# Kernel optimization log

Hardware: AMD Instinct MI355X
Metric: run time of the kernel (lower is better)

Reference implementation:

```python
import jax, jax.numpy as jnp
import numpy as np

NUM_EXPERTS = 8
TOP_K = 2


def setup_inputs() -> dict:
    key = jax.random.key(0)
    k1, k2 = jax.random.split(key)
    N, D = 8192, 4096
    inputs = jax.random.normal(k1, (N, D), dtype=jnp.float32)
    # torch.nn.Linear weight is [out_features, in_features] = [E, D]
    gate_w = jax.random.normal(k2, (NUM_EXPERTS, D), dtype=jnp.float32) * (1.0 / np.sqrt(D))
    return {"inputs": inputs, "gate_w": gate_w}


def reference(inputs, gate_w):
    # gate linear (no bias): [N, D] x [D, E] -> [N, E]
    router_logits = jnp.einsum("nd,ed->ne", inputs.astype(jnp.float32), gate_w)
    router_weights = jax.nn.softmax(router_logits, axis=1)
    # top-k over experts, renormalize selected weights
    sel_w, sel_idx = jax.lax.top_k(router_weights, TOP_K)          # [N, K]
    sel_w = sel_w / jnp.sum(sel_w, axis=-1, keepdims=True)
    # dense equivalent of the per-expert torch.where dispatch:
    # combine[n, e] = renormalized weight of token n for expert e (0 if not selected).
    onehot = jax.nn.one_hot(sel_idx, NUM_EXPERTS, dtype=sel_w.dtype)  # [N, K, E]
    combine = jnp.einsum("nk,nke->ne", sel_w, onehot)               # [N, E]
    return combine, sel_idx
```

## Files before the change

### kernel.cpp

```cpp
#include <hip/hip_runtime.h>
#include <math.h>

#define N_TOK 8192
#define DIM   4096
#define NEXP  8
#define TPW   4
#define HALF  (DIM / 2)
#define ITERS (HALF / 256)
#define WS_NEED ((size_t)N_TOK * 2 * NEXP * sizeof(float))

__global__ __launch_bounds__(256) void router_part_kernel(
    const float* __restrict__ x,
    const float* __restrict__ w,
    float* __restrict__ part)
{
    __shared__ float wl[NEXP][HALF];

    const int tid  = threadIdx.x;
    const int lane = tid & 63;
    const int wid  = tid >> 6;
    const int h    = blockIdx.x & 1;
    const int blk  = blockIdx.x >> 1;
    const int n0   = blk * 16 + wid * TPW;

    {
        const float* wsrc = w + h * HALF;
        #pragma unroll
        for (int e = 0; e < NEXP; ++e) {
            #pragma unroll
            for (int p = 0; p < 2; ++p) {
                const int pos = p * 1024 + tid * 4;
                const float4 v = *(const float4*)(wsrc + (size_t)e * DIM + pos);
                *(float4*)&wl[e][pos] = v;
            }
        }
    }
    __syncthreads();

    const float* xr = x + (size_t)n0 * DIM + h * HALF + lane * 4;
    float4 xq[ITERS][TPW];
    #pragma unroll
    for (int j = 0; j < ITERS; ++j)
        #pragma unroll
        for (int t = 0; t < TPW; ++t)
            xq[j][t] = *(const float4*)(xr + (size_t)t * DIM + j * 256);

    float acc[TPW][NEXP];
    #pragma unroll
    for (int t = 0; t < TPW; ++t)
        #pragma unroll
        for (int e = 0; e < NEXP; ++e) acc[t][e] = 0.0f;

    #pragma unroll
    for (int j = 0; j < ITERS; ++j) {
        float4 wv[NEXP];
        #pragma unroll
        for (int e = 0; e < NEXP; ++e)
            wv[e] = *(const float4*)&wl[e][j * 256 + lane * 4];
        #pragma unroll
        for (int t = 0; t < TPW; ++t) {
            const float4 xv = xq[j][t];
            #pragma unroll
            for (int e = 0; e < NEXP; ++e) {
                acc[t][e] = fmaf(xv.x, wv[e].x,
                            fmaf(xv.y, wv[e].y,
                            fmaf(xv.z, wv[e].z,
                            fmaf(xv.w, wv[e].w, acc[t][e]))));
            }
        }
    }

    #pragma unroll
    for (int t = 0; t < TPW; ++t) {
        #pragma unroll
        for (int e = 0; e < NEXP; ++e) {
            float v = acc[t][e];
            #pragma unroll
            for (int off = 32; off >= 1; off >>= 1)
                v += __shfl_xor(v, off, 64);
            acc[t][e] = v;
        }
    }

    if (lane == 0) {
        #pragma unroll
        for (int t = 0; t < TPW; ++t) {
            float* p = part + ((size_t)(n0 + t) * 2 + h) * NEXP;
            *(float4*)(p + 0) = make_float4(acc[t][0], acc[t][1], acc[t][2], acc[t][3]);
            *(float4*)(p + 4) = make_float4(acc[t][4], acc[t][5], acc[t][6], acc[t][7]);
        }
    }
}

__global__ __launch_bounds__(256) void router_top2_kernel(
    const float* __restrict__ part,
    float* __restrict__ out)
{
    const int n = blockIdx.x * 256 + threadIdx.x;
    const float4* p = (const float4*)(part + (size_t)n * 16);
    const float4 a = p[0], b = p[1];
    const float4 c = p[2], d = p[3];

    float l[NEXP];
    l[0] = a.x + c.x; l[1] = a.y + c.y; l[2] = a.z + c.z; l[3] = a.w + c.w;
    l[4] = b.x + d.x; l[5] = b.y + d.y; l[6] = b.z + d.z; l[7] = b.w + d.w;

    float m1 = l[0]; int i1 = 0;
    #pragma unroll
    for (int e = 1; e < NEXP; ++e)
        if (l[e] > m1) { m1 = l[e]; i1 = e; }
    float m2 = -INFINITY; int i2 = 0;
    #pragma unroll
    for (int e = 0; e < NEXP; ++e)
        if (e != i1 && l[e] > m2) { m2 = l[e]; i2 = e; }

    const float e2  = expf(m2 - m1);
    const float inv = 1.0f / (1.0f + e2);
    const float w1  = inv;
    const float w2  = e2 * inv;

    float cmb[8];
    #pragma unroll
    for (int e = 0; e < 8; ++e)
        cmb[e] = (e == i1) ? w1 : ((e == i2) ? w2 : 0.0f);
    float4* cp = (float4*)(out + (size_t)n * 8);
    cp[0] = make_float4(cmb[0], cmb[1], cmb[2], cmb[3]);
    cp[1] = make_float4(cmb[4], cmb[5], cmb[6], cmb[7]);
    float* ip = out + (size_t)N_TOK * 8 + (size_t)n * 2;
    ip[0] = (float)i1;
    ip[1] = (float)i2;
}

__global__ __launch_bounds__(256) void router_fallback_kernel(
    const float* __restrict__ x, const float* __restrict__ w,
    float* __restrict__ out)
{
    __shared__ float red[2][TPW][NEXP];
    const int lane = threadIdx.x & 63;
    const int wid  = threadIdx.x >> 6;
    const int g    = wid >> 1;
    const int h    = wid & 1;
    const int n0   = blockIdx.x * 8 + g * TPW;

    float acc[TPW][NEXP];
    #pragma unroll
    for (int t = 0; t < TPW; ++t)
        #pragma unroll
        for (int e = 0; e < NEXP; ++e) acc[t][e] = 0.0f;

    const int dbase = h * HALF + lane * 4;
    const float* xr = x + (size_t)n0 * DIM + dbase;
    const float* wr = w + dbase;

    float4 xb[3][TPW];
    #pragma unroll
    for (int t = 0; t < TPW; ++t) xb[0][t] = *(const float4*)(xr + (size_t)t * DIM);
    #pragma unroll
    for (int t = 0; t < TPW; ++t) xb[1][t] = *(const float4*)(xr + (size_t)t * DIM + 256);

    #pragma unroll
    for (int it = 0; it < ITERS; ++it) {
        if (it + 2 < ITERS) {
            const int off = (it + 2) * 256;
            #pragma unroll
            for (int t = 0; t < TPW; ++t)
                xb[(it + 2) % 3][t] = *(const float4*)(xr + (size_t)t * DIM + off);
        }
        float4 wv[NEXP];
        #pragma unroll
        for (int e = 0; e < NEXP; ++e)
            wv[e] = *(const float4*)(wr + (size_t)e * DIM + it * 256);
        #pragma unroll
        for (int t = 0; t < TPW; ++t) {
            const float4 xv = xb[it % 3][t];
            #pragma unroll
            for (int e = 0; e < NEXP; ++e)
                acc[t][e] = fmaf(xv.x, wv[e].x, fmaf(xv.y, wv[e].y,
                            fmaf(xv.z, wv[e].z, fmaf(xv.w, wv[e].w, acc[t][e]))));
        }
    }
    #pragma unroll
    for (int t = 0; t < TPW; ++t)
        #pragma unroll
        for (int e = 0; e < NEXP; ++e) {
            float v = acc[t][e];
            #pragma unroll
            for (int off = 32; off >= 1; off >>= 1) v += __shfl_xor(v, off, 64);
            acc[t][e] = v;
        }
    if (h == 1 && lane == 0) {
        #pragma unroll
        for (int t = 0; t < TPW; ++t) {
            *(float4*)&red[g][t][0] = make_float4(acc[t][0], acc[t][1], acc[t][2], acc[t][3]);
            *(float4*)&red[g][t][4] = make_float4(acc[t][4], acc[t][5], acc[t][6], acc[t][7]);
        }
    }
    __syncthreads();
    if (h == 0) {
        #pragma unroll
        for (int t = 0; t < TPW; ++t) {
            float4 r0 = *(const float4*)&red[g][t][0];
            float4 r1 = *(const float4*)&red[g][t][4];
            acc[t][0] += r0.x; acc[t][1] += r0.y; acc[t][2] += r0.z; acc[t][3] += r0.w;
            acc[t][4] += r1.x; acc[t][5] += r1.y; acc[t][6] += r1.z; acc[t][7] += r1.w;
        }
        #pragma unroll
        for (int t = 0; t < TPW; ++t) {
            float m1 = acc[t][0]; int i1 = 0;
            #pragma unroll
            for (int e = 1; e < NEXP; ++e)
                if (acc[t][e] > m1) { m1 = acc[t][e]; i1 = e; }
            float m2 = -INFINITY; int i2 = 0;
            #pragma unroll
            for (int e = 0; e < NEXP; ++e)
                if (e != i1 && acc[t][e] > m2) { m2 = acc[t][e]; i2 = e; }
            const float e2  = expf(m2 - m1);
            const float inv = 1.0f / (1.0f + e2);
            if (lane == 0) {
                const int n = n0 + t;
                float c[8];
                #pragma unroll
                for (int e = 0; e < 8; ++e)
                    c[e] = (e == i1) ? inv : ((e == i2) ? e2 * inv : 0.0f);
                float4* cp = (float4*)(out + (size_t)n * 8);
                cp[0] = make_float4(c[0], c[1], c[2], c[3]);
                cp[1] = make_float4(c[4], c[5], c[6], c[7]);
                float* ip = out + (size_t)N_TOK * 8 + (size_t)n * 2;
                ip[0] = (float)i1;
                ip[1] = (float)i2;
            }
        }
    }
}

extern "C" void kernel_launch(void* const* d_in, const int* in_sizes, int n_in,
                              void* d_out, int out_size, void* d_ws, size_t ws_size,
                              hipStream_t stream) {
    const float* x = (const float*)d_in[0];
    const float* w = (const float*)d_in[1];
    float* out = (float*)d_out;

    if (ws_size >= WS_NEED) {
        float* part = (float*)d_ws;
        hipLaunchKernelGGL(router_part_kernel, dim3(1024), dim3(256), 0, stream,
                           x, w, part);
        hipLaunchKernelGGL(router_top2_kernel, dim3(N_TOK / 256), dim3(256), 0, stream,
                           part, out);
    } else {
        hipLaunchKernelGGL(router_fallback_kernel, dim3(N_TOK / 8), dim3(256), 0, stream,
                           x, w, out);
    }
}
```

Measured before the change: 33.01 us.

## Split hidden dim into quarters and stream x via direct global-to-LDS ring

The partial-logit kernel now splits the hidden dimension into four quarters instead of two, doubling the grid to 2048 blocks. It loads both weights and x through global_load_lds, staging x in a 3-deep per-wave LDS ring with explicit vmcnt waits, instead of holding all of x in registers. The aim is lower register pressure, more blocks and waves in flight, and x loads that overlap the FMAs. In exchange the workspace and the top-2 kernel must now hold and sum four partials per token, and the hand-counted vmcnt waits are fragile if the compiler adds or reorders memory operations.

```diff
diff --git a/kernel.cpp b/kernel.cpp
--- a/kernel.cpp
+++ b/kernel.cpp
@@ -1,49 +1,59 @@
 #include <hip/hip_runtime.h>
 #include <math.h>
+#include <stdint.h>
 
 #define N_TOK 8192
 #define DIM   4096
 #define NEXP  8
+#define QD    1024
 #define TPW   4
-#define HALF  (DIM / 2)
-#define ITERS (HALF / 256)
-#define WS_NEED ((size_t)N_TOK * 2 * NEXP * sizeof(float))
+#define QITER 4
+#define RING  3
+#define WS_NEED ((size_t)N_TOK * 4 * NEXP * sizeof(float))
+
+__device__ __forceinline__ void glds16(const float* gsrc, const float* lds_base,
+                                       int lds_byte_off_uniform) {
+    __builtin_amdgcn_global_load_lds(
+        (const __attribute__((address_space(1))) uint32_t*)gsrc,
+        (__attribute__((address_space(3))) uint32_t*)((char*)lds_base +
+            __builtin_amdgcn_readfirstlane(lds_byte_off_uniform)),
+        16, 0, 0);
+}
 
 __global__ __launch_bounds__(256) void router_part_kernel(
     const float* __restrict__ x,
     const float* __restrict__ w,
     float* __restrict__ part)
 {
-    __shared__ float wl[NEXP][HALF];
+    __shared__ float wq[NEXP][QD];
+    __shared__ float xl[4][RING][TPW * 256];
 
     const int tid  = threadIdx.x;
     const int lane = tid & 63;
     const int wid  = tid >> 6;
-    const int h    = blockIdx.x & 1;
-    const int blk  = blockIdx.x >> 1;
+    const int q    = blockIdx.x & 3;
+    const int blk  = blockIdx.x >> 2;
     const int n0   = blk * 16 + wid * TPW;
 
     {
-        const float* wsrc = w + h * HALF;
-        #pragma unroll
-        for (int e = 0; e < NEXP; ++e) {
-            #pragma unroll
-            for (int p = 0; p < 2; ++p) {
-                const int pos = p * 1024 + tid * 4;
-                const float4 v = *(const float4*)(wsrc + (size_t)e * DIM + pos);
-                *(float4*)&wl[e][pos] = v;
-            }
+        const float* wg = w + q * QD;
+        #pragma unroll
+        for (int i = 0; i < 8; ++i) {
+            const int f  = wid * 2048 + i * 256;
+            const int e  = f >> 10;
+            const int d0 = f & 1023;
+            glds16(wg + (size_t)e * DIM + d0 + lane * 4, &wq[0][0], f * 4);
         }
     }
     __syncthreads();
 
-    const float* xr = x + (size_t)n0 * DIM + h * HALF + lane * 4;
-    float4 xq[ITERS][TPW];
-    #pragma unroll
-    for (int j = 0; j < ITERS; ++j)
+    const float* xq_ = x + q * QD + lane * 4;
+    #pragma unroll
+    for (int j = 0; j < RING; ++j)
         #pragma unroll
         for (int t = 0; t < TPW; ++t)
-            xq[j][t] = *(const float4*)(xr + (size_t)t * DIM + j * 256);
+            glds16(xq_ + (size_t)(n0 + t) * DIM + j * 256,
+                   &xl[0][0][0], ((wid * RING + j) * 1024 + t * 256) * 4);
 
     float acc[TPW][NEXP];
     #pragma unroll
@@ -52,14 +62,20 @@
         for (int e = 0; e < NEXP; ++e) acc[t][e] = 0.0f;
 
     #pragma unroll
-    for (int j = 0; j < ITERS; ++j) {
+    for (int j = 0; j < QITER; ++j) {
+        if (j <= 1)      { asm volatile("s_waitcnt vmcnt(8)" ::: "memory"); }
+        else if (j == 2) { asm volatile("s_waitcnt vmcnt(4)" ::: "memory"); }
+        else             { asm volatile("s_waitcnt vmcnt(0)" ::: "memory"); }
+        __builtin_amdgcn_sched_barrier(0);
+
         float4 wv[NEXP];
         #pragma unroll
         for (int e = 0; e < NEXP; ++e)
-            wv[e] = *(const float4*)&wl[e][j * 256 + lane * 4];
+            wv[e] = *(const float4*)&wq[e][j * 256 + lane * 4];
+
         #pragma unroll
         for (int t = 0; t < TPW; ++t) {
-            const float4 xv = xq[j][t];
+            const float4 xv = *(const float4*)&xl[wid][j % RING][t * 256 + lane * 4];
             #pragma unroll
             for (int e = 0; e < NEXP; ++e) {
                 acc[t][e] = fmaf(xv.x, wv[e].x,
@@ -68,6 +84,14 @@
                             fmaf(xv.w, wv[e].w, acc[t][e]))));
             }
         }
+
+        if (j + RING < QITER) {
+            #pragma unroll
+            for (int t = 0; t < TPW; ++t)
+                glds16(xq_ + (size_t)(n0 + t) * DIM + (j + RING) * 256,
+                       &xl[0][0][0],
+                       ((wid * RING + (j + RING) % RING) * 1024 + t * 256) * 4);
+        }
     }
 
     #pragma unroll
@@ -85,7 +109,7 @@
     if (lane == 0) {
         #pragma unroll
         for (int t = 0; t < TPW; ++t) {
-            float* p = part + ((size_t)(n0 + t) * 2 + h) * NEXP;
+            float* p = part + ((size_t)(n0 + t) * 4 + q) * NEXP;
             *(float4*)(p + 0) = make_float4(acc[t][0], acc[t][1], acc[t][2], acc[t][3]);
             *(float4*)(p + 4) = make_float4(acc[t][4], acc[t][5], acc[t][6], acc[t][7]);
         }
@@ -97,13 +121,16 @@
     float* __restrict__ out)
 {
     const int n = blockIdx.x * 256 + threadIdx.x;
-    const float4* p = (const float4*)(part + (size_t)n * 16);
-    const float4 a = p[0], b = p[1];
-    const float4 c = p[2], d = p[3];
-
-    float l[NEXP];
-    l[0] = a.x + c.x; l[1] = a.y + c.y; l[2] = a.z + c.z; l[3] = a.w + c.w;
-    l[4] = b.x + d.x; l[5] = b.y + d.y; l[6] = b.z + d.z; l[7] = b.w + d.w;
+    const float4* p = (const float4*)(part + (size_t)n * 32);
+
+    float4 lo = p[0], hi = p[1];
+    #pragma unroll
+    for (int qq = 1; qq < 4; ++qq) {
+        const float4 a = p[qq * 2], b = p[qq * 2 + 1];
+        lo.x += a.x; lo.y += a.y; lo.z += a.z; lo.w += a.w;
+        hi.x += b.x; hi.y += b.y; hi.z += b.z; hi.w += b.w;
+    }
+    float l[NEXP] = {lo.x, lo.y, lo.z, lo.w, hi.x, hi.y, hi.z, hi.w};
 
     float m1 = l[0]; int i1 = 0;
     #pragma unroll
@@ -131,20 +158,23 @@
     ip[1] = (float)i2;
 }
 
+#define TPWF  4
+#define HALF  (DIM / 2)
+#define FITER (HALF / 256)
 __global__ __launch_bounds__(256) void router_fallback_kernel(
     const float* __restrict__ x, const float* __restrict__ w,
     float* __restrict__ out)
 {
-    __shared__ float red[2][TPW][NEXP];
+    __shared__ float red[2][TPWF][NEXP];
     const int lane = threadIdx.x & 63;
     const int wid  = threadIdx.x >> 6;
     const int g    = wid >> 1;
     const int h    = wid & 1;
-    const int n0   = blockIdx.x * 8 + g * TPW;
-
-    float acc[TPW][NEXP];
-    #pragma unroll
-    for (int t = 0; t < TPW; ++t)
+    const int n0   = blockIdx.x * 8 + g * TPWF;
+
+    float acc[TPWF][NEXP];
+    #pragma unroll
+    for (int t = 0; t < TPWF; ++t)
         #pragma unroll
         for (int e = 0; e < NEXP; ++e) acc[t][e] = 0.0f;
 
@@ -152,18 +182,18 @@
     const float* xr = x + (size_t)n0 * DIM + dbase;
     const float* wr = w + dbase;
 
-    float4 xb[3][TPW];
-    #pragma unroll
-    for (int t = 0; t < TPW; ++t) xb[0][t] = *(const float4*)(xr + (size_t)t * DIM);
-    #pragma unroll
-    for (int t = 0; t < TPW; ++t) xb[1][t] = *(const float4*)(xr + (size_t)t * DIM + 256);
-
-    #pragma unroll
-    for (int it = 0; it < ITERS; ++it) {
-        if (it + 2 < ITERS) {
+    float4 xb[3][TPWF];
+    #pragma unroll
+    for (int t = 0; t < TPWF; ++t) xb[0][t] = *(const float4*)(xr + (size_t)t * DIM);
+    #pragma unroll
+    for (int t = 0; t < TPWF; ++t) xb[1][t] = *(const float4*)(xr + (size_t)t * DIM + 256);
+
+    #pragma unroll
+    for (int it = 0; it < FITER; ++it) {
+        if (it + 2 < FITER) {
             const int off = (it + 2) * 256;
             #pragma unroll
-            for (int t = 0; t < TPW; ++t)
+            for (int t = 0; t < TPWF; ++t)
                 xb[(it + 2) % 3][t] = *(const float4*)(xr + (size_t)t * DIM + off);
         }
         float4 wv[NEXP];
@@ -171,7 +201,7 @@
         for (int e = 0; e < NEXP; ++e)
             wv[e] = *(const float4*)(wr + (size_t)e * DIM + it * 256);
         #pragma unroll
-        for (int t = 0; t < TPW; ++t) {
+        for (int t = 0; t < TPWF; ++t) {
             const float4 xv = xb[it % 3][t];
             #pragma unroll
             for (int e = 0; e < NEXP; ++e)
@@ -180,7 +210,7 @@
         }
     }
     #pragma unroll
-    for (int t = 0; t < TPW; ++t)
+    for (int t = 0; t < TPWF; ++t)
         #pragma unroll
         for (int e = 0; e < NEXP; ++e) {
             float v = acc[t][e];
@@ -190,7 +220,7 @@
         }
     if (h == 1 && lane == 0) {
         #pragma unroll
-        for (int t = 0; t < TPW; ++t) {
+        for (int t = 0; t < TPWF; ++t) {
             *(float4*)&red[g][t][0] = make_float4(acc[t][0], acc[t][1], acc[t][2], acc[t][3]);
             *(float4*)&red[g][t][4] = make_float4(acc[t][4], acc[t][5], acc[t][6], acc[t][7]);
         }
@@ -198,14 +228,14 @@
     __syncthreads();
     if (h == 0) {
         #pragma unroll
-        for (int t = 0; t < TPW; ++t) {
+        for (int t = 0; t < TPWF; ++t) {
             float4 r0 = *(const float4*)&red[g][t][0];
             float4 r1 = *(const float4*)&red[g][t][4];
             acc[t][0] += r0.x; acc[t][1] += r0.y; acc[t][2] += r0.z; acc[t][3] += r0.w;
             acc[t][4] += r1.x; acc[t][5] += r1.y; acc[t][6] += r1.z; acc[t][7] += r1.w;
         }
         #pragma unroll
-        for (int t = 0; t < TPW; ++t) {
+        for (int t = 0; t < TPWF; ++t) {
             float m1 = acc[t][0]; int i1 = 0;
             #pragma unroll
             for (int e = 1; e < NEXP; ++e)
@@ -242,7 +272,7 @@
 
     if (ws_size >= WS_NEED) {
         float* part = (float*)d_ws;
-        hipLaunchKernelGGL(router_part_kernel, dim3(1024), dim3(256), 0, stream,
+        hipLaunchKernelGGL(router_part_kernel, dim3(2048), dim3(256), 0, stream,
                            x, w, part);
         hipLaunchKernelGGL(router_top2_kernel, dim3(N_TOK / 256), dim3(256), 0, stream,
                            part, out);
```

After: 40.90 us. +23.9%, slower.
